# Performance work log

Measured on AMD Instinct MI355X. Metric: run time of the kernel, lower is better.

The kernel has to match this reference:

```python
import jax, jax.numpy as jnp
import numpy as np
import math

D_MODEL = 1024
NUM_HEAD = 16


def setup_inputs() -> dict:
    key = jax.random.key(0)
    k1, k2, k3, k4, k5 = jax.random.split(key, 5)
    B, S, D = 4, 2048, D_MODEL
    lim = 1.0 / math.sqrt(D)
    x = jax.random.normal(k1, (B, S, D), dtype=jnp.float32)
    Wqkv = jax.random.uniform(k2, (D, D), jnp.float32, -lim, lim)
    bqkv = jax.random.uniform(k3, (D,), jnp.float32, -lim, lim)
    Wo = jax.random.uniform(k4, (D, D), jnp.float32, -lim, lim)
    bo = jax.random.uniform(k5, (D,), jnp.float32, -lim, lim)
    return {"x": x, "Wqkv": Wqkv, "bqkv": bqkv, "Wo": Wo, "bo": bo}


def reference(x, Wqkv, bqkv, Wo, bo):
    B, S, D = x.shape
    H = NUM_HEAD
    dk = D // H
    # Single shared linear for Q, K, V (qkv_fc applied to x for all three)
    proj = jnp.einsum('bsd,de->bse', x, Wqkv) + bqkv  # [B,S,D]
    # Faithful to source: raw view(B, H, -1, dk) -- reinterprets memory,
    # NOT a head transpose.
    q = proj.reshape(B, H, S, dk)
    k = q
    v = q
    scores = jnp.einsum('bhqd,bhkd->bhqk', q, k) / math.sqrt(dk)  # [B,H,S,S]
    attn = jax.nn.softmax(scores, axis=-1)
    feats = jnp.einsum('bhqk,bhkd->bhqd', attn, v)  # [B,H,S,dk]
    # transpose(1,2) then view(B, -1, H*dk)
    merged = feats.transpose(0, 2, 1, 3).reshape(B, S, H * dk)
    out = jnp.einsum('bsd,de->bse', merged, Wo) + bo
    return out
```

## Files before the change

kernel.cpp:

```cpp
#include <hip/hip_runtime.h>
#include <hip/hip_bf16.h>

typedef __bf16 bf16;
typedef __attribute__((ext_vector_type(8))) __bf16 bf16x8;
typedef __attribute__((ext_vector_type(4))) float f32x4;

#define MFMA_BF16(a, b, c) __builtin_amdgcn_mfma_f32_16x16x32_bf16((a), (b), (c), 0, 0, 0)
#define EXP2F(x) __builtin_amdgcn_exp2f(x)

__device__ __forceinline__ void gload_lds16(const bf16* g, bf16* l) {
  __builtin_amdgcn_global_load_lds(
      (__attribute__((address_space(1))) void*)(g),
      (__attribute__((address_space(3))) void*)(l), 16, 0, 0);
}

__global__ void transcvt2(const float* __restrict__ W0, bf16* __restrict__ T0,
                          const float* __restrict__ W1, bf16* __restrict__ T1) {
  const float* src = blockIdx.z ? W1 : W0;
  bf16* dst = blockIdx.z ? T1 : T0;
  __shared__ float t[32][33];
  const int bx = blockIdx.x * 32, by = blockIdx.y * 32;
  const int tx = threadIdx.x, ty = threadIdx.y;
#pragma unroll
  for (int i = 0; i < 4; ++i)
    t[ty + i * 8][tx] = src[(long)(by + ty + i * 8) * 1024 + bx + tx];
  __syncthreads();
#pragma unroll
  for (int i = 0; i < 4; ++i)
    dst[(long)(bx + ty + i * 8) * 1024 + by + tx] = (bf16)t[tx][ty + i * 8];
}

template <bool A_IS_F32, bool OUT_F32>
__global__ __launch_bounds__(256) void gemm_bt(const void* __restrict__ Av,
                                               const bf16* __restrict__ Bt,
                                               const float* __restrict__ bias,
                                               void* __restrict__ Cv) {
  __shared__ __align__(16) bf16 As[128 * 32];
  __shared__ __align__(16) bf16 Bs[128 * 32];
  const int tid = threadIdx.x;
  const int l = tid & 63, w = tid >> 6;
  const int wr = w >> 1, wc = w & 1;
  const int lo = l & 15, g = l >> 4;
  const int m0 = blockIdx.x * 128;
  const int n0 = blockIdx.y * 128;
  const bf16* Ab = (const bf16*)Av + (long)m0 * 1024;
  const float* Af = (const float*)Av + (long)m0 * 1024;
  const bf16* Bb = Bt + (long)n0 * 1024;
  const int srow = tid >> 2;
  const int schunk = (tid & 3) * 8;
  f32x4 acc[4][4] = {};
  for (int k0 = 0; k0 < 1024; k0 += 32) {
    __syncthreads();
    if constexpr (A_IS_F32) {
#pragma unroll
      for (int h = 0; h < 2; ++h) {
        const float* p = Af + (long)(srow + h * 64) * 1024 + k0 + schunk;
        f32x4 u0 = *(const f32x4*)p;
        f32x4 u1 = *(const f32x4*)(p + 4);
        bf16x8 vv;
#pragma unroll
        for (int e = 0; e < 4; ++e) {
          vv[e] = (bf16)u0[e];
          vv[4 + e] = (bf16)u1[e];
        }
        *(bf16x8*)&As[h * 2048 + tid * 8] = vv;
      }
    } else {
      gload_lds16(Ab + (long)srow * 1024 + k0 + schunk, As + tid * 8);
      gload_lds16(Ab + (long)(srow + 64) * 1024 + k0 + schunk, As + 2048 + tid * 8);
    }
    gload_lds16(Bb + (long)srow * 1024 + k0 + schunk, Bs + tid * 8);
    gload_lds16(Bb + (long)(srow + 64) * 1024 + k0 + schunk, Bs + 2048 + tid * 8);
    __syncthreads();
    bf16x8 af[4], bfr[4];
#pragma unroll
    for (int m = 0; m < 4; ++m)
      af[m] = *(const bf16x8*)&As[(wr * 64 + m * 16 + lo) * 32 + g * 8];
#pragma unroll
    for (int n = 0; n < 4; ++n)
      bfr[n] = *(const bf16x8*)&Bs[(wc * 64 + n * 16 + lo) * 32 + g * 8];
#pragma unroll
    for (int m = 0; m < 4; ++m)
#pragma unroll
      for (int n = 0; n < 4; ++n)
        acc[m][n] = MFMA_BF16(af[m], bfr[n], acc[m][n]);
  }
#pragma unroll
  for (int n = 0; n < 4; ++n) {
    const int col = n0 + wc * 64 + n * 16 + lo;
    const float bv = bias[col];
#pragma unroll
    for (int m = 0; m < 4; ++m) {
      const long row0 = m0 + wr * 64 + m * 16 + g * 4;
#pragma unroll
      for (int j = 0; j < 4; ++j) {
        if constexpr (OUT_F32)
          ((float*)Cv)[(row0 + j) * 1024 + col] = acc[m][n][j] + bv;
        else
          ((bf16*)Cv)[(row0 + j) * 1024 + col] = (bf16)(acc[m][n][j] + bv);
      }
    }
  }
}

__global__ __launch_bounds__(256) void attn(const bf16* __restrict__ proj,
                                            bf16* __restrict__ merged) {
  __shared__ __align__(16) bf16 Vt[64][66];
  __shared__ __align__(16) bf16 Plds[4][32][66];
  const int bid = blockIdx.x;
  const int qb = bid & 15;
  const int h = (bid >> 4) & 15;
  const int b = bid >> 8;
  const bf16* P = proj + (long)b * 2097152 + (long)h * 131072;
  const int tid = threadIdx.x;
  const int w = tid >> 6, l = tid & 63;
  const int lo = l & 15, g = l >> 4;
  const int qrow = qb * 128 + w * 32;

  const float QSCALE = 0.125f * 1.44269504088896f;
  bf16x8 qa[2][2];
#pragma unroll
  for (int m = 0; m < 2; ++m)
#pragma unroll
    for (int ks = 0; ks < 2; ++ks) {
      bf16x8 t = *(const bf16x8*)&P[(long)(qrow + m * 16 + lo) * 64 + ks * 32 + g * 8];
#pragma unroll
      for (int e = 0; e < 8; ++e) t[e] = (bf16)((float)t[e] * QSCALE);
      qa[m][ks] = t;
    }

  f32x4 o[2][4] = {};
  float mq[2] = {-1e30f, -1e30f};
  float lq[2] = {0.f, 0.f};

  const int skv = tid >> 3;
  const int sc = tid & 7;

  for (int kv0 = 0; kv0 < 2048; kv0 += 64) {
    __syncthreads();
#pragma unroll
    for (int it = 0; it < 2; ++it) {
      const int kv = skv + it * 32;
      bf16x8 v = *(const bf16x8*)&P[(long)(kv0 + kv) * 64 + sc * 8];
#pragma unroll
      for (int e = 0; e < 8; ++e) Vt[sc * 8 + e][kv] = v[e];
    }
    __syncthreads();

    f32x4 s[2][4] = {};
#pragma unroll
    for (int kt = 0; kt < 4; ++kt)
#pragma unroll
      for (int ks = 0; ks < 2; ++ks) {
        bf16x8 kb = *(const bf16x8*)&P[(long)(kv0 + kt * 16 + lo) * 64 + ks * 32 + g * 8];
        s[0][kt] = MFMA_BF16(kb, qa[0][ks], s[0][kt]);
        s[1][kt] = MFMA_BF16(kb, qa[1][ks], s[1][kt]);
      }

#pragma unroll
    for (int m = 0; m < 2; ++m) {
      float mx = -1e30f;
#pragma unroll
      for (int kt = 0; kt < 4; ++kt)
#pragma unroll
        for (int j = 0; j < 4; ++j) mx = fmaxf(mx, s[m][kt][j]);
      mx = fmaxf(mx, __shfl_xor(mx, 16));
      mx = fmaxf(mx, __shfl_xor(mx, 32));
      const float mnew = fmaxf(mq[m], mx);
      const float corr = EXP2F(mq[m] - mnew);
      mq[m] = mnew;
      float ps = 0.f;
#pragma unroll
      for (int kt = 0; kt < 4; ++kt)
#pragma unroll
        for (int j = 0; j < 4; ++j) {
          const float p = EXP2F(s[m][kt][j] - mnew);
          s[m][kt][j] = p;
          ps += p;
        }
      ps += __shfl_xor(ps, 16);
      ps += __shfl_xor(ps, 32);
      lq[m] = lq[m] * corr + ps;
#pragma unroll
      for (int kt = 0; kt < 4; ++kt)
#pragma unroll
        for (int j = 0; j < 4; ++j)
          Plds[w][m * 16 + lo][(((kt * 2 + (g >> 1)) ^ (lo & 3)) << 3) + ((g & 1) << 2) + j] =
              (bf16)s[m][kt][j];
#pragma unroll
      for (int j = 0; j < 4; ++j) {
        const float cj = __shfl(corr, g * 4 + j, 16);
#pragma unroll
        for (int n = 0; n < 4; ++n) o[m][n][j] *= cj;
      }
    }

#pragma unroll
    for (int ks = 0; ks < 2; ++ks) {
      const int pc = ((ks * 4 + g) ^ (lo & 3)) << 3;
      bf16x8 pa0 = *(const bf16x8*)&Plds[w][lo][pc];
      bf16x8 pa1 = *(const bf16x8*)&Plds[w][16 + lo][pc];
#pragma unroll
      for (int n = 0; n < 4; ++n) {
        bf16x8 vb = *(const bf16x8*)&Vt[n * 16 + lo][ks * 32 + g * 8];
        o[0][n] = MFMA_BF16(pa0, vb, o[0][n]);
        o[1][n] = MFMA_BF16(pa1, vb, o[1][n]);
      }
    }
  }

  bf16* mb = merged + (long)b * 2097152 + h * 64;
#pragma unroll
  for (int m = 0; m < 2; ++m)
#pragma unroll
    for (int j = 0; j < 4; ++j) {
      const float lj = __shfl(lq[m], g * 4 + j, 16);
      const float inv = 1.0f / lj;
      const int sq = qrow + m * 16 + g * 4 + j;
#pragma unroll
      for (int n = 0; n < 4; ++n)
        mb[(long)sq * 1024 + n * 16 + lo] = (bf16)(o[m][n][j] * inv);
    }
}

extern "C" void kernel_launch(void* const* d_in, const int* in_sizes, int n_in,
                              void* d_out, int out_size, void* d_ws, size_t ws_size,
                              hipStream_t stream) {
  const float* x = (const float*)d_in[0];
  const float* Wqkv = (const float*)d_in[1];
  const float* bqkv = (const float*)d_in[2];
  const float* Wo = (const float*)d_in[3];
  const float* bo = (const float*)d_in[4];
  float* out = (float*)d_out;

  char* ws = (char*)d_ws;
  bf16* proj = (bf16*)(ws);
  bf16* merged = (bf16*)(ws + 16777216);
  bf16* WqkvT = (bf16*)(ws + 33554432);
  bf16* WoT = (bf16*)(ws + 35651584);

  transcvt2<<<dim3(32, 32, 2), dim3(32, 8), 0, stream>>>(Wqkv, WqkvT, Wo, WoT);
  gemm_bt<true, false><<<dim3(64, 8), dim3(256), 0, stream>>>(x, WqkvT, bqkv, proj);
  attn<<<dim3(1024), dim3(256), 0, stream>>>(proj, merged);
  gemm_bt<false, true><<<dim3(64, 8), dim3(256), 0, stream>>>(merged, WoT, bo, out);
}
```

Baseline: 343.8 us.

## Rewrite attention with 32x32 MFMA, register-resident P, and double-buffered K/V prefetch

Rewrites the attention kernel to use 32x32x16 bf16 MFMAs with scores computed transposed, so each lane owns one query row. The probabilities are packed to bf16 and exchanged across half-waves with shuffles instead of going through LDS. K fragments and the next V tile are prefetched one step ahead into double buffers. The online-softmax rescale is skipped when no lane's max increases. This is meant to remove the LDS round trip for P, the cross-lane reductions and the load stalls. In exchange it takes on register pressure and intricate lane-layout logic, plus a barrier every 32-key step.

```diff
diff --git a/kernel.cpp b/kernel.cpp
--- a/kernel.cpp
+++ b/kernel.cpp
@@ -4,14 +4,22 @@
 typedef __bf16 bf16;
 typedef __attribute__((ext_vector_type(8))) __bf16 bf16x8;
 typedef __attribute__((ext_vector_type(4))) float f32x4;
+typedef __attribute__((ext_vector_type(16))) float f32x16;
 
 #define MFMA_BF16(a, b, c) __builtin_amdgcn_mfma_f32_16x16x32_bf16((a), (b), (c), 0, 0, 0)
+#define MFMA32(a, b, c) __builtin_amdgcn_mfma_f32_32x32x16_bf16((a), (b), (c), 0, 0, 0)
 #define EXP2F(x) __builtin_amdgcn_exp2f(x)
 
 __device__ __forceinline__ void gload_lds16(const bf16* g, bf16* l) {
   __builtin_amdgcn_global_load_lds(
       (__attribute__((address_space(1))) void*)(g),
       (__attribute__((address_space(3))) void*)(l), 16, 0, 0);
+}
+
+__device__ __forceinline__ int cvtpk(float lo, float hi) {
+  int r;
+  asm("v_cvt_pk_bf16_f32 %0, %1, %2" : "=v"(r) : "v"(lo), "v"(hi));
+  return r;
 }
 
 __global__ void transcvt2(const float* __restrict__ W0, bf16* __restrict__ T0,
@@ -105,122 +113,136 @@
 
 __global__ __launch_bounds__(256) void attn(const bf16* __restrict__ proj,
                                             bf16* __restrict__ merged) {
-  __shared__ __align__(16) bf16 Vt[64][66];
-  __shared__ __align__(16) bf16 Plds[4][32][66];
+  __shared__ __align__(16) bf16 Vt[2][64][34];
   const int bid = blockIdx.x;
   const int qb = bid & 15;
-  const int h = (bid >> 4) & 15;
+  const int hh = (bid >> 4) & 15;
   const int b = bid >> 8;
-  const bf16* P = proj + (long)b * 2097152 + (long)h * 131072;
+  const bf16* P = proj + (long)b * 2097152 + (long)hh * 131072;
   const int tid = threadIdx.x;
   const int w = tid >> 6, l = tid & 63;
-  const int lo = l & 15, g = l >> 4;
+  const int l31 = l & 31;
+  const bool hi = (l >= 32);
+  const int hf = hi ? 1 : 0;
   const int qrow = qb * 128 + w * 32;
 
+  const int skv = tid >> 3;
+  const int sc = (tid & 7) * 8;
+
   const float QSCALE = 0.125f * 1.44269504088896f;
-  bf16x8 qa[2][2];
-#pragma unroll
-  for (int m = 0; m < 2; ++m)
-#pragma unroll
-    for (int ks = 0; ks < 2; ++ks) {
-      bf16x8 t = *(const bf16x8*)&P[(long)(qrow + m * 16 + lo) * 64 + ks * 32 + g * 8];
-#pragma unroll
-      for (int e = 0; e < 8; ++e) t[e] = (bf16)((float)t[e] * QSCALE);
-      qa[m][ks] = t;
+  bf16x8 qf[4];
+#pragma unroll
+  for (int s = 0; s < 4; ++s) {
+    bf16x8 t = *(const bf16x8*)&P[(long)(qrow + l31) * 64 + s * 16 + hf * 8];
+#pragma unroll
+    for (int e = 0; e < 8; ++e) t[e] = (bf16)((float)t[e] * QSCALE);
+    qf[s] = t;
+  }
+
+  f32x16 o0 = {}, o1 = {};
+  float mq = -1e30f, lq = 0.f;
+
+  bf16x8 kA[4], kB[4];
+  {
+    bf16x8 v = *(const bf16x8*)&P[(long)skv * 64 + sc];
+#pragma unroll
+    for (int e = 0; e < 8; ++e) Vt[0][sc + e][skv] = v[e];
+  }
+#pragma unroll
+  for (int s = 0; s < 4; ++s)
+    kA[s] = *(const bf16x8*)&P[(long)l31 * 64 + s * 16 + hf * 8];
+  __syncthreads();
+
+  for (int t2 = 0; t2 < 32; ++t2) {
+#pragma unroll
+    for (int ph = 0; ph < 2; ++ph) {
+      const int t = t2 * 2 + ph;
+      const int tn = (t < 63) ? t + 1 : 63;
+      bf16x8 vnx = *(const bf16x8*)&P[((long)tn * 32 + skv) * 64 + sc];
+      f32x16 s;
+      if (ph == 0) {
+        s = MFMA32(kA[0], qf[0], f32x16{});
+        s = MFMA32(kA[1], qf[1], s);
+        s = MFMA32(kA[2], qf[2], s);
+        s = MFMA32(kA[3], qf[3], s);
+      } else {
+        s = MFMA32(kB[0], qf[0], f32x16{});
+        s = MFMA32(kB[1], qf[1], s);
+        s = MFMA32(kB[2], qf[2], s);
+        s = MFMA32(kB[3], qf[3], s);
+      }
+#pragma unroll
+      for (int sx = 0; sx < 4; ++sx) {
+        bf16x8 kv8 = *(const bf16x8*)&P[((long)tn * 32 + l31) * 64 + sx * 16 + hf * 8];
+        if (ph == 0) kB[sx] = kv8; else kA[sx] = kv8;
+      }
+      float mx = s[0];
+#pragma unroll
+      for (int i = 1; i < 16; ++i) mx = fmaxf(mx, s[i]);
+      mx = fmaxf(mx, __shfl_xor(mx, 32));
+      if (__any(mx > mq)) {
+        const float mnew = fmaxf(mq, mx);
+        const float corr = EXP2F(mq - mnew);
+        mq = mnew;
+        lq *= corr;
+#pragma unroll
+        for (int i = 0; i < 16; ++i) { o0[i] *= corr; o1[i] *= corr; }
+      }
+      float ps = 0.f;
+#pragma unroll
+      for (int i = 0; i < 16; ++i) {
+        const float p = EXP2F(s[i] - mq);
+        s[i] = p;
+        ps += p;
+      }
+      ps += __shfl_xor(ps, 32);
+      lq += ps;
+      const int pk0 = cvtpk(s[0], s[1]), pk1 = cvtpk(s[2], s[3]);
+      const int pk2 = cvtpk(s[4], s[5]), pk3 = cvtpk(s[6], s[7]);
+      const int pk4 = cvtpk(s[8], s[9]), pk5 = cvtpk(s[10], s[11]);
+      const int pk6 = cvtpk(s[12], s[13]), pk7 = cvtpk(s[14], s[15]);
+      const int x0 = __shfl_xor(pk0, 32), x2 = __shfl_xor(pk2, 32);
+      const int x1 = __shfl_xor(pk1, 32), x3 = __shfl_xor(pk3, 32);
+      const int x4 = __shfl_xor(pk4, 32), x6 = __shfl_xor(pk6, 32);
+      const int x5 = __shfl_xor(pk5, 32), x7 = __shfl_xor(pk7, 32);
+      int bi0[4], bi1[4];
+      bi0[0] = hi ? x2 : pk0;
+      bi0[1] = hi ? x3 : pk1;
+      bi0[2] = hi ? pk2 : x0;
+      bi0[3] = hi ? pk3 : x1;
+      bi1[0] = hi ? x6 : pk4;
+      bi1[1] = hi ? x7 : pk5;
+      bi1[2] = hi ? pk6 : x4;
+      bi1[3] = hi ? pk7 : x5;
+      bf16x8 pb0 = *(bf16x8*)bi0;
+      bf16x8 pb1 = *(bf16x8*)bi1;
+      {
+        bf16x8 va;
+        va = *(const bf16x8*)&Vt[ph][l31][hf * 8];
+        o0 = MFMA32(va, pb0, o0);
+        va = *(const bf16x8*)&Vt[ph][l31][16 + hf * 8];
+        o0 = MFMA32(va, pb1, o0);
+        va = *(const bf16x8*)&Vt[ph][32 + l31][hf * 8];
+        o1 = MFMA32(va, pb0, o1);
+        va = *(const bf16x8*)&Vt[ph][32 + l31][16 + hf * 8];
+        o1 = MFMA32(va, pb1, o1);
+      }
+#pragma unroll
+      for (int e = 0; e < 8; ++e) Vt[ph ^ 1][sc + e][skv] = vnx[e];
+      __syncthreads();
     }
-
-  f32x4 o[2][4] = {};
-  float mq[2] = {-1e30f, -1e30f};
-  float lq[2] = {0.f, 0.f};
-
-  const int skv = tid >> 3;
-  const int sc = tid & 7;
-
-  for (int kv0 = 0; kv0 < 2048; kv0 += 64) {
-    __syncthreads();
-#pragma unroll
-    for (int it = 0; it < 2; ++it) {
-      const int kv = skv + it * 32;
-      bf16x8 v = *(const bf16x8*)&P[(long)(kv0 + kv) * 64 + sc * 8];
-#pragma unroll
-      for (int e = 0; e < 8; ++e) Vt[sc * 8 + e][kv] = v[e];
-    }
-    __syncthreads();
-
-    f32x4 s[2][4] = {};
-#pragma unroll
-    for (int kt = 0; kt < 4; ++kt)
-#pragma unroll
-      for (int ks = 0; ks < 2; ++ks) {
-        bf16x8 kb = *(const bf16x8*)&P[(long)(kv0 + kt * 16 + lo) * 64 + ks * 32 + g * 8];
-        s[0][kt] = MFMA_BF16(kb, qa[0][ks], s[0][kt]);
-        s[1][kt] = MFMA_BF16(kb, qa[1][ks], s[1][kt]);
-      }
-
-#pragma unroll
-    for (int m = 0; m < 2; ++m) {
-      float mx = -1e30f;
-#pragma unroll
-      for (int kt = 0; kt < 4; ++kt)
-#pragma unroll
-        for (int j = 0; j < 4; ++j) mx = fmaxf(mx, s[m][kt][j]);
-      mx = fmaxf(mx, __shfl_xor(mx, 16));
-      mx = fmaxf(mx, __shfl_xor(mx, 32));
-      const float mnew = fmaxf(mq[m], mx);
-      const float corr = EXP2F(mq[m] - mnew);
-      mq[m] = mnew;
-      float ps = 0.f;
-#pragma unroll
-      for (int kt = 0; kt < 4; ++kt)
-#pragma unroll
-        for (int j = 0; j < 4; ++j) {
-          const float p = EXP2F(s[m][kt][j] - mnew);
-          s[m][kt][j] = p;
-          ps += p;
-        }
-      ps += __shfl_xor(ps, 16);
-      ps += __shfl_xor(ps, 32);
-      lq[m] = lq[m] * corr + ps;
-#pragma unroll
-      for (int kt = 0; kt < 4; ++kt)
-#pragma unroll
-        for (int j = 0; j < 4; ++j)
-          Plds[w][m * 16 + lo][(((kt * 2 + (g >> 1)) ^ (lo & 3)) << 3) + ((g & 1) << 2) + j] =
-              (bf16)s[m][kt][j];
-#pragma unroll
-      for (int j = 0; j < 4; ++j) {
-        const float cj = __shfl(corr, g * 4 + j, 16);
-#pragma unroll
-        for (int n = 0; n < 4; ++n) o[m][n][j] *= cj;
-      }
-    }
-
-#pragma unroll
-    for (int ks = 0; ks < 2; ++ks) {
-      const int pc = ((ks * 4 + g) ^ (lo & 3)) << 3;
-      bf16x8 pa0 = *(const bf16x8*)&Plds[w][lo][pc];
-      bf16x8 pa1 = *(const bf16x8*)&Plds[w][16 + lo][pc];
-#pragma unroll
-      for (int n = 0; n < 4; ++n) {
-        bf16x8 vb = *(const bf16x8*)&Vt[n * 16 + lo][ks * 32 + g * 8];
-        o[0][n] = MFMA_BF16(pa0, vb, o[0][n]);
-        o[1][n] = MFMA_BF16(pa1, vb, o[1][n]);
-      }
-    }
-  }
-
-  bf16* mb = merged + (long)b * 2097152 + h * 64;
-#pragma unroll
-  for (int m = 0; m < 2; ++m)
-#pragma unroll
-    for (int j = 0; j < 4; ++j) {
-      const float lj = __shfl(lq[m], g * 4 + j, 16);
-      const float inv = 1.0f / lj;
-      const int sq = qrow + m * 16 + g * 4 + j;
-#pragma unroll
-      for (int n = 0; n < 4; ++n)
-        mb[(long)sq * 1024 + n * 16 + lo] = (bf16)(o[m][n][j] * inv);
-    }
+  }
+
+  const float inv = 1.0f / lq;
+  bf16* mb = merged + (long)b * 2097152 + hh * 64;
+  const long rowoff = (long)(qrow + l31) * 1024;
+  const int dbase[8] = {0, 2, 8, 10, 16, 18, 24, 26};
+#pragma unroll
+  for (int r = 0; r < 8; ++r) {
+    const int d = dbase[r] + 4 * hf;
+    *(int*)&mb[rowoff + d] = cvtpk(o0[2 * r] * inv, o0[2 * r + 1] * inv);
+    *(int*)&mb[rowoff + 32 + d] = cvtpk(o1[2 * r] * inv, o1[2 * r + 1] * inv);
+  }
 }
 
 extern "C" void kernel_launch(void* const* d_in, const int* in_sizes, int n_in,
```

Result: faster. 327.0 us (-4.9%).
